# Kernel optimization log

Hardware: AMD Instinct MI355X
Metric: run time of the kernel (lower is better)

The kernel has to match this reference:

```python
import jax, jax.numpy as jnp
import numpy as np

N, D, DPE, H = 4096, 256, 16, 8
HD = D // H
SCALE = HD ** -0.5


def setup_inputs() -> dict:
    key = jax.random.key(0)
    ks = jax.random.split(key, 10)
    s = lambda fan_in: 1.0 / np.sqrt(fan_in)
    return {
        "x": jax.random.normal(ks[0], (N, D), jnp.float32),
        "pe": jax.random.normal(ks[1], (N, DPE), jnp.float32),
        "Wqkv": jax.random.uniform(ks[2], (D, 3 * D), jnp.float32, -s(D), s(D)),
        "bqkv": jax.random.uniform(ks[3], (3 * D,), jnp.float32, -s(D), s(D)),
        "Wpe": jax.random.uniform(ks[4], (DPE, H), jnp.float32, -s(DPE), s(DPE)),
        "bpe": jax.random.uniform(ks[5], (H,), jnp.float32, -s(DPE), s(DPE)),
        "Wout": jax.random.uniform(ks[6], (D, D), jnp.float32, -s(D), s(D)),
        "bout": jax.random.uniform(ks[7], (D,), jnp.float32, -s(D), s(D)),
    }


def reference(x, pe, Wqkv, bqkv, Wpe, bpe, Wout, bout):
    # qkv: [N, 3, H, HD] -> q,k,v each [H, N, HD]
    qkv = (x @ Wqkv + bqkv).reshape(N, 3, H, HD).transpose(1, 2, 0, 3)
    q, k, v = qkv[0], qkv[1], qkv[2]
    # attention scores [H, N, N]
    attn = jnp.einsum("hnd,hmd->hnm", q, k) * SCALE
    # pairwise PE-difference bias: bias[h,i,j] = pe_proj[i,h] - pe_proj[j,h]
    pe_proj = pe @ Wpe + bpe  # [N, H]
    pe_bias = (pe_proj[:, None, :] - pe_proj[None, :, :]).transpose(2, 0, 1)
    attn = jax.nn.softmax(attn + pe_bias, axis=-1)
    # dropout disabled (eval mode, p=0)
    out = jnp.einsum("hnm,hmd->nhd", attn, v).reshape(N, D)
    return out @ Wout + bout
```

## Files before the change

kernel.cpp:

```cpp
#include <hip/hip_runtime.h>
#include <math.h>

#define NN 4096
#define HH 8
constexpr float SCALE = 0.17677669529663687f;
constexpr float LOG2E = 1.4426950408889634f;
constexpr float SC2   = SCALE * LOG2E;

typedef __bf16 bf16;
typedef __bf16 bf16x8 __attribute__((ext_vector_type(8)));
typedef __bf16 bf16x4 __attribute__((ext_vector_type(4)));
typedef float  f32x4  __attribute__((ext_vector_type(4)));

#define MFMA(a, b, c) __builtin_amdgcn_mfma_f32_16x16x32_bf16((a), (b), (c), 0, 0, 0)

template <int K, int N, bool SCALEQ>
__device__ __forceinline__ void wcast_body(const float* __restrict__ W,
                                           bf16* __restrict__ WhT,
                                           bf16* __restrict__ WlT,
                                           int n0, int k0, int t,
                                           float (*tile)[65]) {
#pragma unroll
    for (int p = 0; p < 16; ++p) {
        const int r = p * 4 + (t >> 6);
        const int c = t & 63;
        tile[r][c] = W[(size_t)(k0 + r) * N + n0 + c];
    }
    __syncthreads();
    const int nr = t >> 2, kc0 = (t & 3) * 16;
    const float sc = (SCALEQ && (n0 + nr) < 256) ? SC2 : 1.0f;
    bf16x8 h[2], l[2];
#pragma unroll
    for (int g = 0; g < 2; ++g)
#pragma unroll
        for (int j = 0; j < 8; ++j) {
            const float v = tile[kc0 + g * 8 + j][nr] * sc;
            const bf16 hh = (bf16)v;
            h[g][j] = hh;
            l[g][j] = (bf16)(v - (float)hh);
        }
    const size_t ob = (size_t)(n0 + nr) * K + k0 + kc0;
    *(bf16x8*)&WhT[ob] = h[0];
    *(bf16x8*)&WhT[ob + 8] = h[1];
    *(bf16x8*)&WlT[ob] = l[0];
    *(bf16x8*)&WlT[ob + 8] = l[1];
}

__global__ __launch_bounds__(256) void preproc_kernel(
    const float* __restrict__ Wqkv, const float* __restrict__ Wout,
    const float* __restrict__ bqkv, const float* __restrict__ pe,
    const float* __restrict__ Wpe, const float* __restrict__ bpe,
    bf16* __restrict__ WqkvhT, bf16* __restrict__ WqkvlT,
    bf16* __restrict__ WouthT, bf16* __restrict__ WoutlT,
    float* __restrict__ bqkv_s, float* __restrict__ ep) {
    __shared__ float tile[64][65];
    const int b = blockIdx.x, t = threadIdx.x;
    if (b < 48) {
        wcast_body<256, 768, true>(Wqkv, WqkvhT, WqkvlT, (b % 12) * 64, (b / 12) * 64, t, tile);
    } else if (b < 64) {
        const int bb = b - 48;
        wcast_body<256, 256, false>(Wout, WouthT, WoutlT, (bb % 4) * 64, (bb / 4) * 64, t, tile);
    } else if (b < 192) {
        const int idx = (b - 64) * 256 + t;
        const int h = idx >> 12;
        const int n = idx & 4095;
        float acc = bpe[h];
#pragma unroll
        for (int k = 0; k < 16; ++k) acc += pe[n * 16 + k] * Wpe[k * 8 + h];
        ep[h * NN + n] = __builtin_amdgcn_exp2f(-acc * LOG2E - 8.0f);
    } else {
        for (int i = t; i < 768; i += 256)
            bqkv_s[i] = bqkv[i] * (i < 256 ? SC2 : 1.0f);
    }
}

template <int NOUT, int NTILE, typename OT>
__global__ __launch_bounds__(256, 2) void gemm3x_kernel(const float* __restrict__ A,
                                                        const bf16* __restrict__ BhT,
                                                        const bf16* __restrict__ BlT,
                                                        const float* __restrict__ bias,
                                                        OT* __restrict__ C) {
    constexpr int NS = NTILE / 16;
    const int t = threadIdx.x, wave = t >> 6, lane = t & 63;
    const int quad = lane >> 4, i16 = lane & 15;
    const int m0 = blockIdx.x * 128 + wave * 32;
    const int n0 = blockIdx.y * NTILE;

    __shared__ __align__(16) bf16 Bs[NTILE * 512];

    {
        const int l = t & 63, i16l = l & 15, ql = l >> 4;
#pragma unroll
        for (int c = t >> 6; c < NS * 16; c += 4) {
            const bool lo = c >= NS * 8;
            const int cc = lo ? c - NS * 8 : c;
            const int nsi = cc >> 3, kc = cc & 7;
            const bf16* src = (lo ? BlT : BhT) +
                (size_t)(n0 + nsi * 16 + i16l) * 256 + kc * 32 + ql * 8;
            *(uint4*)&Bs[c * 512 + l * 8] = *(const uint4*)src;
        }
    }

    bf16x8 ah[2][8], al[2][8];
#pragma unroll
    for (int ms = 0; ms < 2; ++ms) {
        const int row = m0 + ms * 16 + i16;
#pragma unroll
        for (int kc = 0; kc < 8; ++kc) {
            const size_t ab = (size_t)row * 256 + kc * 32 + quad * 8;
            const f32x4 u0 = *(const f32x4*)&A[ab];
            const f32x4 u1 = *(const f32x4*)&A[ab + 4];
#pragma unroll
            for (int e = 0; e < 4; ++e) {
                const bf16 h0 = (bf16)u0[e], h1 = (bf16)u1[e];
                ah[ms][kc][e] = h0;
                ah[ms][kc][e + 4] = h1;
                al[ms][kc][e] = (bf16)(u0[e] - (float)h0);
                al[ms][kc][e + 4] = (bf16)(u1[e] - (float)h1);
            }
        }
    }
    __syncthreads();

#pragma unroll
    for (int nsi = 0; nsi < NS; ++nsi) {
        f32x4 acc[2];
        acc[0] = f32x4{0.f, 0.f, 0.f, 0.f};
        acc[1] = f32x4{0.f, 0.f, 0.f, 0.f};
#pragma unroll
        for (int kc = 0; kc < 8; ++kc) {
            const bf16x8 bh = *(const bf16x8*)&Bs[(nsi * 8 + kc) * 512 + lane * 8];
            const bf16x8 bl = *(const bf16x8*)&Bs[((NS + nsi) * 8 + kc) * 512 + lane * 8];
            acc[0] = MFMA(ah[0][kc], bh, acc[0]);
            acc[0] = MFMA(ah[0][kc], bl, acc[0]);
            acc[0] = MFMA(al[0][kc], bh, acc[0]);
            acc[1] = MFMA(ah[1][kc], bh, acc[1]);
            acc[1] = MFMA(ah[1][kc], bl, acc[1]);
            acc[1] = MFMA(al[1][kc], bh, acc[1]);
        }
        const int n = n0 + nsi * 16 + i16;
        const float b = bias[n];
#pragma unroll
        for (int ms = 0; ms < 2; ++ms)
#pragma unroll
            for (int r = 0; r < 4; ++r)
                C[(size_t)(m0 + ms * 16 + quad * 4 + r) * NOUT + n] = (OT)(acc[ms][r] + b);
    }
}

template <int NOUT, int NTILE, typename OT>
__global__ __launch_bounds__(256, 2) void gemm3s_kernel(const bf16* __restrict__ Ah,
                                                        const bf16* __restrict__ Al,
                                                        const bf16* __restrict__ BhT,
                                                        const bf16* __restrict__ BlT,
                                                        const float* __restrict__ bias,
                                                        OT* __restrict__ C) {
    constexpr int NS = NTILE / 16;
    const int t = threadIdx.x, wave = t >> 6, lane = t & 63;
    const int quad = lane >> 4, i16 = lane & 15;
    const int m0 = blockIdx.x * 128 + wave * 32;
    const int n0 = blockIdx.y * NTILE;

    __shared__ __align__(16) bf16 Bs[NTILE * 512];

    {
        const int l = t & 63, i16l = l & 15, ql = l >> 4;
#pragma unroll
        for (int c = t >> 6; c < NS * 16; c += 4) {
            const bool lo = c >= NS * 8;
            const int cc = lo ? c - NS * 8 : c;
            const int nsi = cc >> 3, kc = cc & 7;
            const bf16* src = (lo ? BlT : BhT) +
                (size_t)(n0 + nsi * 16 + i16l) * 256 + kc * 32 + ql * 8;
            *(uint4*)&Bs[c * 512 + l * 8] = *(const uint4*)src;
        }
    }

    bf16x8 ah[2][8], al[2][8];
#pragma unroll
    for (int ms = 0; ms < 2; ++ms) {
        const size_t abase = (size_t)(m0 + ms * 16 + i16) * 256 + quad * 8;
#pragma unroll
        for (int kc = 0; kc < 8; ++kc) {
            ah[ms][kc] = *(const bf16x8*)&Ah[abase + kc * 32];
            al[ms][kc] = *(const bf16x8*)&Al[abase + kc * 32];
        }
    }
    __syncthreads();

#pragma unroll
    for (int nsi = 0; nsi < NS; ++nsi) {
        f32x4 acc[2];
        acc[0] = f32x4{0.f, 0.f, 0.f, 0.f};
        acc[1] = f32x4{0.f, 0.f, 0.f, 0.f};
#pragma unroll
        for (int kc = 0; kc < 8; ++kc) {
            const bf16x8 bh = *(const bf16x8*)&Bs[(nsi * 8 + kc) * 512 + lane * 8];
            const bf16x8 bl = *(const bf16x8*)&Bs[((NS + nsi) * 8 + kc) * 512 + lane * 8];
            acc[0] = MFMA(ah[0][kc], bh, acc[0]);
            acc[0] = MFMA(ah[0][kc], bl, acc[0]);
            acc[0] = MFMA(al[0][kc], bh, acc[0]);
            acc[1] = MFMA(ah[1][kc], bh, acc[1]);
            acc[1] = MFMA(ah[1][kc], bl, acc[1]);
            acc[1] = MFMA(al[1][kc], bh, acc[1]);
        }
        const int n = n0 + nsi * 16 + i16;
        const float b = bias[n];
#pragma unroll
        for (int ms = 0; ms < 2; ++ms)
#pragma unroll
            for (int r = 0; r < 4; ++r)
                C[(size_t)(m0 + ms * 16 + quad * 4 + r) * NOUT + n] = (OT)(acc[ms][r] + b);
    }
}

__global__ __launch_bounds__(256) void kvtrans_kernel(const bf16* __restrict__ qkvb,
                                                      const float* __restrict__ ep,
                                                      bf16* __restrict__ Kf,
                                                      bf16* __restrict__ Vf) {
    const int t = threadIdx.x;
    const int kt = blockIdx.y, h = blockIdx.x;
    __shared__ __align__(16) bf16 Ktile[64 * 32];
    __shared__ __align__(16) bf16 Vtile[64 * 32];
    __shared__ float eps[64];
    {
        const int tok = kt * 64 + (t >> 2);
        const int d8 = (t & 3) * 8;
        *(uint4*)&Ktile[(t >> 2) * 32 + d8] =
            *(const uint4*)&qkvb[(size_t)tok * 768 + 256 + h * 32 + d8];
        *(uint4*)&Vtile[(t >> 2) * 32 + d8] =
            *(const uint4*)&qkvb[(size_t)tok * 768 + 512 + h * 32 + d8];
        if (t < 64) eps[t] = ep[h * NN + kt * 64 + t];
    }
    __syncthreads();
    {
        const int s = t >> 6, l = t & 63, quad = l >> 4, i16 = l & 15;
        bf16x8 o;
#pragma unroll
        for (int j = 0; j < 8; ++j) o[j] = Ktile[(s * 16 + i16) * 32 + quad * 8 + j];
        *(bf16x8*)&Kf[((size_t)(h * 64 + kt) * 4 + s) * 512 + l * 8] = o;
    }
    for (int c = t; c < 384; c += 256) {
        const int ch = c >> 6, ll = c & 63, qd = ll >> 4, ii = ll & 15;
        const int dt = ch >> 1, kc = ch & 1;
        const int dimp = dt * 16 + ii;
        bf16x8 o;
#pragma unroll
        for (int j = 0; j < 8; ++j) {
            const int key = kc * 32 + qd * 8 + j;
            float v;
            if (dimp < 32)       v = (float)Vtile[key * 32 + dimp] * eps[key];
            else if (dimp == 32) v = eps[key];
            else                 v = 0.f;
            o[j] = (bf16)v;
        }
        *(bf16x8*)&Vf[((size_t)(h * 64 + kt) * 6 + ch) * 512 + ll * 8] = o;
    }
}

__global__ __launch_bounds__(512, 4) void attn_kernel(const bf16* __restrict__ qkvb,
                                                      const bf16* __restrict__ Kf,
                                                      const bf16* __restrict__ Vf,
                                                      bf16* __restrict__ aoh,
                                                      bf16* __restrict__ aol) {
    const int t = threadIdx.x, w = t >> 6, lane = t & 63;
    const int quad = lane >> 4, i16 = lane & 15;
    const int qb = blockIdx.y, h = blockIdx.x;

    __shared__ __align__(16) bf16 Pt[8][4][16 * 72];

    const int q0 = qb * 64;
    bf16x8 qf[4];
#pragma unroll
    for (int qs = 0; qs < 4; ++qs)
        qf[qs] = *(const bf16x8*)&qkvb[(size_t)(q0 + qs * 16 + i16) * 768 + h * 32 + quad * 8];

    f32x4 o[3][4];
#pragma unroll
    for (int dt = 0; dt < 3; ++dt)
#pragma unroll
        for (int qs = 0; qs < 4; ++qs) o[dt][qs] = f32x4{0.f, 0.f, 0.f, 0.f};

    const bf16* kb = Kf + (size_t)(h * 64) * 2048 + lane * 8;
    const bf16* vb = Vf + (size_t)(h * 64) * 3072 + lane * 8;

    const int kt0 = w * 8;
    for (int it = 0; it < 8; ++it) {
        const int kt = kt0 + it;
        bf16x8 kcur[4];
#pragma unroll
        for (int s = 0; s < 4; ++s)
            kcur[s] = *(const bf16x8*)&kb[((size_t)kt * 4 + s) * 512];

        const f32x4 z = {0.f, 0.f, 0.f, 0.f};
#pragma unroll
        for (int qh = 0; qh < 2; ++qh) {
            f32x4 sf[2][4];
#pragma unroll
            for (int ks = 0; ks < 4; ++ks) {
                sf[0][ks] = MFMA(kcur[ks], qf[qh * 2 + 0], z);
                sf[1][ks] = MFMA(kcur[ks], qf[qh * 2 + 1], z);
            }
#pragma unroll
            for (int qi = 0; qi < 2; ++qi) {
                const int qs = qh * 2 + qi;
#pragma unroll
                for (int ks = 0; ks < 4; ++ks) {
                    bf16x4 pk;
#pragma unroll
                    for (int r = 0; r < 4; ++r)
                        pk[r] = (bf16)__builtin_amdgcn_exp2f(sf[qi][ks][r]);
                    *(bf16x4*)&Pt[w][qs][i16 * 72 + ks * 16 + quad * 4] = pk;
                }
            }
        }

        bf16x8 vv[6];
#pragma unroll
        for (int c = 0; c < 6; ++c)
            vv[c] = *(const bf16x8*)&vb[((size_t)kt * 6 + c) * 512];
        asm volatile("s_waitcnt lgkmcnt(0)" ::: "memory");

#pragma unroll
        for (int qs = 0; qs < 4; ++qs) {
            const bf16x8 pb0 = *(const bf16x8*)&Pt[w][qs][i16 * 72 + 0 * 32 + quad * 8];
            const bf16x8 pb1 = *(const bf16x8*)&Pt[w][qs][i16 * 72 + 1 * 32 + quad * 8];
#pragma unroll
            for (int dt = 0; dt < 3; ++dt) {
                o[dt][qs] = MFMA(vv[dt * 2 + 0], pb0, o[dt][qs]);
                o[dt][qs] = MFMA(vv[dt * 2 + 1], pb1, o[dt][qs]);
            }
        }
    }

    {
        float* myo = (float*)&Pt[w][0][0];
#pragma unroll
        for (int qs = 0; qs < 4; ++qs) {
            *(f32x4*)&myo[(qs * 64 + lane) * 8 + 0] = o[0][qs];
            *(f32x4*)&myo[(qs * 64 + lane) * 8 + 4] = o[1][qs];
        }
        if (quad == 0) {
#pragma unroll
            for (int qs = 0; qs < 4; ++qs)
                myo[2048 + qs * 16 + i16] = o[2][qs][0];
        }
    }
    __syncthreads();
    if (w < 4) {
        f32x4 a0 = {0.f, 0.f, 0.f, 0.f}, a1 = {0.f, 0.f, 0.f, 0.f};
        float lsum = 0.f;
#pragma unroll
        for (int ww = 0; ww < 8; ++ww) {
            const float* p = (const float*)&Pt[ww][0][0];
            a0 += *(const f32x4*)&p[(w * 64 + lane) * 8 + 0];
            a1 += *(const f32x4*)&p[(w * 64 + lane) * 8 + 4];
            if (lane < 16) lsum += p[2048 + w * 16 + lane];
        }
        const float linv = 1.0f / __shfl(lsum, i16, 64);
        const int row = q0 + w * 16 + i16;
#pragma unroll
        for (int dt = 0; dt < 2; ++dt) {
            const f32x4 src = dt ? a1 : a0;
            bf16x4 hi, lo;
#pragma unroll
            for (int r = 0; r < 4; ++r) {
                const float v = src[r] * linv;
                hi[r] = (bf16)v;
                lo[r] = (bf16)(v - (float)hi[r]);
            }
            const size_t ob = (size_t)row * 256 + h * 32 + dt * 16 + quad * 4;
            *(bf16x4*)&aoh[ob] = hi;
            *(bf16x4*)&aol[ob] = lo;
        }
    }
}

extern "C" void kernel_launch(void* const* d_in, const int* in_sizes, int n_in,
                              void* d_out, int out_size, void* d_ws, size_t ws_size,
                              hipStream_t stream) {
    const float* x    = (const float*)d_in[0];
    const float* pe   = (const float*)d_in[1];
    const float* Wqkv = (const float*)d_in[2];
    const float* bqkv = (const float*)d_in[3];
    const float* Wpe  = (const float*)d_in[4];
    const float* bpe  = (const float*)d_in[5];
    const float* Wout = (const float*)d_in[6];
    const float* bout = (const float*)d_in[7];
    float* out = (float*)d_out;

    char* ws = (char*)d_ws;
    bf16*  WqkvhT  = (bf16*)(ws);
    bf16*  WqkvlT  = (bf16*)(ws + 393216);
    bf16*  WouthT  = (bf16*)(ws + 786432);
    bf16*  WoutlT  = (bf16*)(ws + 917504);
    float* bqkv_s  = (float*)(ws + 1048576);
    bf16*  qkvb    = (bf16*)(ws + 1051648);
    float* ep      = (float*)(ws + 7343104);
    bf16*  Kf      = (bf16*)(ws + 7474176);
    bf16*  Vf      = (bf16*)(ws + 9571328);
    bf16*  aoh     = (bf16*)(ws + 12717056);
    bf16*  aol     = (bf16*)(ws + 14814208);

    preproc_kernel<<<193, 256, 0, stream>>>(Wqkv, Wout, bqkv, pe, Wpe, bpe,
                                            WqkvhT, WqkvlT, WouthT, WoutlT,
                                            bqkv_s, ep);
    gemm3x_kernel<768, 48, bf16><<<dim3(32, 16), 256, 0, stream>>>(x, WqkvhT, WqkvlT, bqkv_s, qkvb);
    kvtrans_kernel<<<dim3(HH, 64), 256, 0, stream>>>(qkvb, ep, Kf, Vf);
    attn_kernel<<<dim3(HH, NN / 64), 512, 0, stream>>>(qkvb, Kf, Vf, aoh, aol);
    gemm3s_kernel<256, 16, float><<<dim3(32, 16), 256, 0, stream>>>(aoh, aol, WouthT, WoutlT, bout, out);
}
```

Baseline: 129.9 us.

## Fuse K/V transpose and PE scaling into QKV projection GEMM epilogue

The QKV GEMM now uses 32-column tiles aligned to one head's Q, K or V slice. Q blocks write a compact Q buffer, while K and V blocks stage the tile in shared memory and write the MFMA-ready Kf/Vf layouts directly, including the exp(PE) scaling of V. This removes the separate kvtrans kernel launch and the round trip of K and V through global memory. In exchange the GEMM grid grows, each block carries a smaller tile, and it adds an extra shared-memory barrier and epilogue work.

Result: no change. 127.8 us (-1.6%).

```diff
diff --git a/kernel.cpp b/kernel.cpp
--- a/kernel.cpp
+++ b/kernel.cpp
@@ -74,32 +74,34 @@
     }
 }
 
-template <int NOUT, int NTILE, typename OT>
-__global__ __launch_bounds__(256, 2) void gemm3x_kernel(const float* __restrict__ A,
-                                                        const bf16* __restrict__ BhT,
-                                                        const bf16* __restrict__ BlT,
-                                                        const float* __restrict__ bias,
-                                                        OT* __restrict__ C) {
-    constexpr int NS = NTILE / 16;
+__global__ __launch_bounds__(256, 2) void gemmqkv_kernel(
+    const float* __restrict__ A, const bf16* __restrict__ BhT,
+    const bf16* __restrict__ BlT, const float* __restrict__ bias,
+    const float* __restrict__ ep,
+    bf16* __restrict__ Qb, bf16* __restrict__ Kf, bf16* __restrict__ Vf) {
     const int t = threadIdx.x, wave = t >> 6, lane = t & 63;
     const int quad = lane >> 4, i16 = lane & 15;
-    const int m0 = blockIdx.x * 128 + wave * 32;
-    const int n0 = blockIdx.y * NTILE;
-
-    __shared__ __align__(16) bf16 Bs[NTILE * 512];
+    const int mb = blockIdx.x, ct = blockIdx.y;
+    const int m0 = mb * 128 + wave * 32;
+    const int n0 = ct * 32;
+
+    __shared__ __align__(16) bf16 Bs[32 * 512];
+    __shared__ __align__(16) bf16 Ctl[128 * 36];
+    __shared__ float eps[128];
 
     {
-        const int l = t & 63, i16l = l & 15, ql = l >> 4;
-#pragma unroll
-        for (int c = t >> 6; c < NS * 16; c += 4) {
-            const bool lo = c >= NS * 8;
-            const int cc = lo ? c - NS * 8 : c;
+        const int i16l = lane & 15, ql = lane >> 4;
+#pragma unroll
+        for (int c = wave; c < 32; c += 4) {
+            const bool lo = c >= 16;
+            const int cc = lo ? c - 16 : c;
             const int nsi = cc >> 3, kc = cc & 7;
             const bf16* src = (lo ? BlT : BhT) +
                 (size_t)(n0 + nsi * 16 + i16l) * 256 + kc * 32 + ql * 8;
-            *(uint4*)&Bs[c * 512 + l * 8] = *(const uint4*)src;
-        }
-    }
+            *(uint4*)&Bs[c * 512 + lane * 8] = *(const uint4*)src;
+        }
+    }
+    if (ct >= 16 && t < 128) eps[t] = ep[(ct - 16) * NN + mb * 128 + t];
 
     bf16x8 ah[2][8], al[2][8];
 #pragma unroll
@@ -122,29 +124,82 @@
     }
     __syncthreads();
 
-#pragma unroll
-    for (int nsi = 0; nsi < NS; ++nsi) {
-        f32x4 acc[2];
-        acc[0] = f32x4{0.f, 0.f, 0.f, 0.f};
-        acc[1] = f32x4{0.f, 0.f, 0.f, 0.f};
+    f32x4 acc[2][2];
+#pragma unroll
+    for (int nsi = 0; nsi < 2; ++nsi) {
+        acc[nsi][0] = f32x4{0.f, 0.f, 0.f, 0.f};
+        acc[nsi][1] = f32x4{0.f, 0.f, 0.f, 0.f};
 #pragma unroll
         for (int kc = 0; kc < 8; ++kc) {
             const bf16x8 bh = *(const bf16x8*)&Bs[(nsi * 8 + kc) * 512 + lane * 8];
-            const bf16x8 bl = *(const bf16x8*)&Bs[((NS + nsi) * 8 + kc) * 512 + lane * 8];
-            acc[0] = MFMA(ah[0][kc], bh, acc[0]);
-            acc[0] = MFMA(ah[0][kc], bl, acc[0]);
-            acc[0] = MFMA(al[0][kc], bh, acc[0]);
-            acc[1] = MFMA(ah[1][kc], bh, acc[1]);
-            acc[1] = MFMA(ah[1][kc], bl, acc[1]);
-            acc[1] = MFMA(al[1][kc], bh, acc[1]);
-        }
+            const bf16x8 bl = *(const bf16x8*)&Bs[((2 + nsi) * 8 + kc) * 512 + lane * 8];
+            acc[nsi][0] = MFMA(ah[0][kc], bh, acc[nsi][0]);
+            acc[nsi][0] = MFMA(ah[0][kc], bl, acc[nsi][0]);
+            acc[nsi][0] = MFMA(al[0][kc], bh, acc[nsi][0]);
+            acc[nsi][1] = MFMA(ah[1][kc], bh, acc[nsi][1]);
+            acc[nsi][1] = MFMA(ah[1][kc], bl, acc[nsi][1]);
+            acc[nsi][1] = MFMA(al[1][kc], bh, acc[nsi][1]);
+        }
+    }
+
+    if (ct < 8) {
+#pragma unroll
+        for (int nsi = 0; nsi < 2; ++nsi) {
+            const int n = n0 + nsi * 16 + i16;
+            const float b = bias[n];
+#pragma unroll
+            for (int ms = 0; ms < 2; ++ms)
+#pragma unroll
+                for (int r = 0; r < 4; ++r)
+                    Qb[(size_t)(m0 + ms * 16 + quad * 4 + r) * 256 + n] =
+                        (bf16)(acc[nsi][ms][r] + b);
+        }
+        return;
+    }
+
+#pragma unroll
+    for (int nsi = 0; nsi < 2; ++nsi) {
         const int n = n0 + nsi * 16 + i16;
         const float b = bias[n];
 #pragma unroll
         for (int ms = 0; ms < 2; ++ms)
 #pragma unroll
             for (int r = 0; r < 4; ++r)
-                C[(size_t)(m0 + ms * 16 + quad * 4 + r) * NOUT + n] = (OT)(acc[ms][r] + b);
+                Ctl[(wave * 32 + ms * 16 + quad * 4 + r) * 36 + nsi * 16 + i16] =
+                    (bf16)(acc[nsi][ms][r] + b);
+    }
+    __syncthreads();
+
+    if (ct < 16) {
+        const int h = ct - 8;
+#pragma unroll
+        for (int c = wave; c < 8; c += 4) {
+            const int half = c >> 2, s = c & 3;
+            bf16x8 o;
+#pragma unroll
+            for (int j = 0; j < 8; ++j)
+                o[j] = Ctl[(half * 64 + s * 16 + i16) * 36 + quad * 8 + j];
+            *(bf16x8*)&Kf[((size_t)(h * 64 + mb * 2 + half) * 4 + s) * 512 + lane * 8] = o;
+        }
+    } else {
+        const int h = ct - 16;
+#pragma unroll
+        for (int c = wave; c < 12; c += 4) {
+            const int half = c / 6, ch = c % 6;
+            const int dt = ch >> 1, kc = ch & 1;
+            const int dimp = dt * 16 + i16;
+            bf16x8 o;
+#pragma unroll
+            for (int j = 0; j < 8; ++j) {
+                const int key = half * 64 + kc * 32 + quad * 8 + j;
+                float v;
+                if (dimp < 32)       v = (float)Ctl[key * 36 + dimp] * eps[key];
+                else if (dimp == 32) v = eps[key];
+                else                 v = 0.f;
+                o[j] = (bf16)v;
+            }
+            *(bf16x8*)&Vf[((size_t)(h * 64 + mb * 2 + half) * 6 + ch) * 512 + lane * 8] = o;
+        }
     }
 }
 
@@ -214,51 +269,7 @@
     }
 }
 
-__global__ __launch_bounds__(256) void kvtrans_kernel(const bf16* __restrict__ qkvb,
-                                                      const float* __restrict__ ep,
-                                                      bf16* __restrict__ Kf,
-                                                      bf16* __restrict__ Vf) {
-    const int t = threadIdx.x;
-    const int kt = blockIdx.y, h = blockIdx.x;
-    __shared__ __align__(16) bf16 Ktile[64 * 32];
-    __shared__ __align__(16) bf16 Vtile[64 * 32];
-    __shared__ float eps[64];
-    {
-        const int tok = kt * 64 + (t >> 2);
-        const int d8 = (t & 3) * 8;
-        *(uint4*)&Ktile[(t >> 2) * 32 + d8] =
-            *(const uint4*)&qkvb[(size_t)tok * 768 + 256 + h * 32 + d8];
-        *(uint4*)&Vtile[(t >> 2) * 32 + d8] =
-            *(const uint4*)&qkvb[(size_t)tok * 768 + 512 + h * 32 + d8];
-        if (t < 64) eps[t] = ep[h * NN + kt * 64 + t];
-    }
-    __syncthreads();
-    {
-        const int s = t >> 6, l = t & 63, quad = l >> 4, i16 = l & 15;
-        bf16x8 o;
-#pragma unroll
-        for (int j = 0; j < 8; ++j) o[j] = Ktile[(s * 16 + i16) * 32 + quad * 8 + j];
-        *(bf16x8*)&Kf[((size_t)(h * 64 + kt) * 4 + s) * 512 + l * 8] = o;
-    }
-    for (int c = t; c < 384; c += 256) {
-        const int ch = c >> 6, ll = c & 63, qd = ll >> 4, ii = ll & 15;
-        const int dt = ch >> 1, kc = ch & 1;
-        const int dimp = dt * 16 + ii;
-        bf16x8 o;
-#pragma unroll
-        for (int j = 0; j < 8; ++j) {
-            const int key = kc * 32 + qd * 8 + j;
-            float v;
-            if (dimp < 32)       v = (float)Vtile[key * 32 + dimp] * eps[key];
-            else if (dimp == 32) v = eps[key];
-            else                 v = 0.f;
-            o[j] = (bf16)v;
-        }
-        *(bf16x8*)&Vf[((size_t)(h * 64 + kt) * 6 + ch) * 512 + ll * 8] = o;
-    }
-}
-
-__global__ __launch_bounds__(512, 4) void attn_kernel(const bf16* __restrict__ qkvb,
+__global__ __launch_bounds__(512, 4) void attn_kernel(const bf16* __restrict__ Qb,
                                                       const bf16* __restrict__ Kf,
                                                       const bf16* __restrict__ Vf,
                                                       bf16* __restrict__ aoh,
@@ -273,7 +284,7 @@
     bf16x8 qf[4];
 #pragma unroll
     for (int qs = 0; qs < 4; ++qs)
-        qf[qs] = *(const bf16x8*)&qkvb[(size_t)(q0 + qs * 16 + i16) * 768 + h * 32 + quad * 8];
+        qf[qs] = *(const bf16x8*)&Qb[(size_t)(q0 + qs * 16 + i16) * 256 + h * 32 + quad * 8];
 
     f32x4 o[3][4];
 #pragma unroll
@@ -395,18 +406,18 @@
     bf16*  WouthT  = (bf16*)(ws + 786432);
     bf16*  WoutlT  = (bf16*)(ws + 917504);
     float* bqkv_s  = (float*)(ws + 1048576);
-    bf16*  qkvb    = (bf16*)(ws + 1051648);
-    float* ep      = (float*)(ws + 7343104);
-    bf16*  Kf      = (bf16*)(ws + 7474176);
-    bf16*  Vf      = (bf16*)(ws + 9571328);
-    bf16*  aoh     = (bf16*)(ws + 12717056);
-    bf16*  aol     = (bf16*)(ws + 14814208);
+    float* ep      = (float*)(ws + 1051648);
+    bf16*  Qb      = (bf16*)(ws + 1182720);
+    bf16*  Kf      = (bf16*)(ws + 3279872);
+    bf16*  Vf      = (bf16*)(ws + 5377024);
+    bf16*  aoh     = (bf16*)(ws + 8522752);
+    bf16*  aol     = (bf16*)(ws + 10619904);
 
     preproc_kernel<<<193, 256, 0, stream>>>(Wqkv, Wout, bqkv, pe, Wpe, bpe,
                                             WqkvhT, WqkvlT, WouthT, WoutlT,
                                             bqkv_s, ep);
-    gemm3x_kernel<768, 48, bf16><<<dim3(32, 16), 256, 0, stream>>>(x, WqkvhT, WqkvlT, bqkv_s, qkvb);
-    kvtrans_kernel<<<dim3(HH, 64), 256, 0, stream>>>(qkvb, ep, Kf, Vf);
-    attn_kernel<<<dim3(HH, NN / 64), 512, 0, stream>>>(qkvb, Kf, Vf, aoh, aol);
+    gemmqkv_kernel<<<dim3(32, 24), 256, 0, stream>>>(x, WqkvhT, WqkvlT, bqkv_s, ep,
+                                                     Qb, Kf, Vf);
+    attn_kernel<<<dim3(HH, NN / 64), 512, 0, stream>>>(Qb, Kf, Vf, aoh, aol);
     gemm3s_kernel<256, 16, float><<<dim3(32, 16), 256, 0, stream>>>(aoh, aol, WouthT, WoutlT, bout, out);
 }
```
